# Kernel tuning notes

Hardware: AMD Instinct MI355X
Metric: run time of the kernel (lower is better)

The kernel has to match this reference:

```python
import jax, jax.numpy as jnp
import numpy as np

N = 50000      # nodes
E = 800000     # edges (avg degree 16)
D = 128        # hidden dim
L = 3          # message-passing layers
NU = 1         # DRew nu -> delay = max(k - nu, 0)


def setup_inputs() -> dict:
    key = jax.random.key(0)
    ks = jax.random.split(key, 6)
    x = jax.random.normal(ks[0], (N, D), dtype=jnp.float32)
    edge_index = jax.random.randint(ks[1], (2, E), 0, N)          # [2, E] (src, dst)
    edge_attr = jax.random.randint(ks[2], (E,), 1, L + 1)          # edge types in {1..L}
    scale = 1.0 / np.sqrt(D).astype(np.float32)
    Ws = jax.random.normal(ks[3], (L, D, D), dtype=jnp.float32) * scale       # mlp_s per layer
    bs = jnp.zeros((L, D), dtype=jnp.float32)
    Wk = jax.random.normal(ks[4], (L, L, D, D), dtype=jnp.float32) * scale    # mlp_k, padded; layer t uses k=1..t+1
    bk = jnp.zeros((L, L, D), dtype=jnp.float32)
    eps = jnp.zeros((L,), dtype=jnp.float32)
    return dict(x=x, edge_index=edge_index, edge_attr=edge_attr,
                Ws=Ws, bs=bs, Wk=Wk, bk=bk, eps=eps)


def reference(x, edge_index, edge_attr, Ws, bs, Wk, bk, eps):
    src, dst = edge_index[0], edge_index[1]
    xs = [x]
    for t in range(L):
        xt = xs[-1]
        # out = (1 + eps) * mlp_s(x)
        out = (1.0 + eps[t]) * jax.nn.relu(xt @ Ws[t] + bs[t])
        for k in range(1, t + 2):
            delay = max(k - NU, 0)
            x_src = xs[t - delay]                       # delayed node features
            mask = (edge_attr == k).astype(xt.dtype)    # edge-type mask (replaces boolean column select)
            msg = x_src[src] * mask[:, None]            # gather + mask: [E, D]
            agg = jax.ops.segment_sum(msg, dst, num_segments=N)  # scatter-add per destination
            out = out + jax.nn.relu(agg @ Wk[t, k - 1] + bk[t, k - 1])  # mlp_k(k)
        # gin_nn_post is an empty Sequential -> identity; then F.relu; then residual
        h = jax.nn.relu(out)
        xs.append(xt + h)
    return xs[-1]
```

## Files before the change

kernel.cpp:

```cpp
#include <hip/hip_runtime.h>
#include <hip/hip_bf16.h>


#define NODES 50000
#define EDGES 800000
#define DIM   128
#define ND    ((long)NODES * DIM)
#define NB3   (3 * NODES)
#define NPART 4
#define PSIZE (NODES / NPART)
#define NROWP 50048
#define NBLKS ((NB3 + 255) / 256)

typedef __attribute__((ext_vector_type(8))) short  bf16x8;
typedef __attribute__((ext_vector_type(4))) float  f32x4;

#define LDS_STRIDE 136

__global__ __launch_bounds__(256) void init_kernel(
    const float* __restrict__ x, const float* __restrict__ Ws,
    const float* __restrict__ Wk, __hip_bfloat16* __restrict__ xb0,
    __hip_bfloat16* __restrict__ xb1, __hip_bfloat16* __restrict__ xb2,
    __hip_bfloat16* __restrict__ WT, int* __restrict__ cursor) {
  int b = blockIdx.x, tid = threadIdx.x;
  long i = (long)b * 256 + tid;
  if (i < ND / 4) {
    float4 v = ((const float4*)x)[i];
    union { __hip_bfloat16 h[4]; uint2 u; } pk;
    pk.h[0] = __float2bfloat16(v.x); pk.h[1] = __float2bfloat16(v.y);
    pk.h[2] = __float2bfloat16(v.z); pk.h[3] = __float2bfloat16(v.w);
    ((uint2*)xb0)[i] = pk.u;
  }
  if (b < 12) {
    const float* src = (b < 3) ? (Ws + (long)b * 16384) : (Wk + (long)(b - 3) * 16384);
    __hip_bfloat16* dst = WT + (long)b * 16384;
    for (int idx = tid; idx < 16384; idx += 256) {
      int k = idx >> 7, n = idx & 127;
      dst[n * 128 + k] = __float2bfloat16(src[idx]);
    }
  }
  if (b >= 12 && b < 12 + NBLKS) {
    int g = (b - 12) * 256 + tid;
    if (g < NB3) cursor[g] = 0;
  }
  if (b == 599 && tid < DIM) {
    xb0[(long)NODES * DIM + tid] = __float2bfloat16(0.f);
    xb1[(long)NODES * DIM + tid] = __float2bfloat16(0.f);
    xb2[(long)NODES * DIM + tid] = __float2bfloat16(0.f);
  }
}

__global__ __launch_bounds__(256) void hist_kernel(
    const int* __restrict__ ei, const int* __restrict__ attr,
    int* __restrict__ counts, int E) {
  int e = blockIdx.x * 256 + threadIdx.x;
  if (e >= E) return;
  atomicAdd(&counts[(attr[e] - 1) * NODES + ei[E + e]], 1);
}

__global__ __launch_bounds__(256) void scan_a_kernel(
    const int* __restrict__ counts, int* __restrict__ partial,
    int* __restrict__ blocksums, int n) {
  __shared__ int tmp[256];
  int gid = blockIdx.x * 256 + threadIdx.x;
  int v = (gid < n) ? ((counts[gid] + 3) & ~3) : 0;
  tmp[threadIdx.x] = v;
  __syncthreads();
  for (int off = 1; off < 256; off <<= 1) {
    int t = (threadIdx.x >= off) ? tmp[threadIdx.x - off] : 0;
    __syncthreads();
    tmp[threadIdx.x] += t;
    __syncthreads();
  }
  if (gid < n) partial[gid] = tmp[threadIdx.x] - v;
  if (threadIdx.x == 255) blocksums[blockIdx.x] = tmp[255];
}

__global__ __launch_bounds__(256) void scanc_kernel(
    int* __restrict__ rowptr, int* __restrict__ cursor,
    const int* __restrict__ blocksums, int* __restrict__ csr, int n) {
  __shared__ int red[256];
  int tid = threadIdx.x;
  int partial = 0;
  for (int i = tid; i < blockIdx.x; i += 256) partial += blocksums[i];
  red[tid] = partial;
  __syncthreads();
  for (int off = 128; off > 0; off >>= 1) {
    if (tid < off) red[tid] += red[tid + off];
    __syncthreads();
  }
  int bsoff = red[0];
  int gid = blockIdx.x * 256 + tid;
  if (gid < n) {
    int cnt = cursor[gid];
    int pcnt = (cnt + 3) & ~3;
    int val = rowptr[gid] + bsoff;
    rowptr[gid] = val;
    cursor[gid] = val;
    for (int i = cnt; i < pcnt; ++i) csr[val + i] = NODES;
    if (gid == n - 1) rowptr[n] = val + pcnt;
  }
}

__global__ __launch_bounds__(256) void fill_kernel(
    const int* __restrict__ ei, const int* __restrict__ attr,
    int* __restrict__ cursor, int* __restrict__ csr_src, int E) {
  int p = blockIdx.x & (NPART - 1);
  int chunk = blockIdx.x >> 2;
  int e = chunk * 256 + threadIdx.x;
  if (e >= E) return;
  int d = ei[E + e];
  int lo = p * PSIZE;
  if (d < lo || d >= lo + PSIZE) return;
  int pos = atomicAdd(&cursor[(attr[e] - 1) * NODES + d], 1);
  csr_src[pos] = ei[e];
}

__global__ __launch_bounds__(256, 6) void gather_kernel(
    const __hip_bfloat16* __restrict__ src,
    const int* __restrict__ rowptr, const int* __restrict__ csr,
    __hip_bfloat16* __restrict__ ag0, __hip_bfloat16* __restrict__ ag1,
    __hip_bfloat16* __restrict__ ag2, int nwork) {
  int group = (blockIdx.x * 256 + threadIdx.x) >> 4;
  int lane16 = threadIdx.x & 15;
  if (group >= nwork) return;
  int km1 = (group >= 2 * NODES) ? 2 : ((group >= NODES) ? 1 : 0);
  int d = group - km1 * NODES;
  __hip_bfloat16* ag = (km1 == 0) ? ag0 : ((km1 == 1) ? ag1 : ag2);
  int beg = rowptr[group], end = rowptr[group + 1];
  float a0 = 0.f, a1 = 0.f, a2 = 0.f, a3 = 0.f,
        a4 = 0.f, a5 = 0.f, a6 = 0.f, a7 = 0.f;
  for (int base = beg; base < end; base += 16) {
    int idxv = csr[base + lane16];
    int cnt = end - base; if (cnt > 16) cnt = 16;
    int q0 = __shfl(idxv, 0, 16);
    int q1 = __shfl(idxv, 1, 16);
    int q2 = __shfl(idxv, 2, 16);
    int q3 = __shfl(idxv, 3, 16);
    uint4 v0 = *(const uint4*)(src + (long)q0 * DIM + lane16 * 8);
    uint4 v1 = *(const uint4*)(src + (long)q1 * DIM + lane16 * 8);
    uint4 v2 = *(const uint4*)(src + (long)q2 * DIM + lane16 * 8);
    uint4 v3 = *(const uint4*)(src + (long)q3 * DIM + lane16 * 8);
    for (int j = 0; j < cnt; j += 4) {
      uint4 c0 = v0, c1 = v1, c2 = v2, c3 = v3;
      if (j + 4 < cnt) {
        q0 = __shfl(idxv, j + 4, 16);
        q1 = __shfl(idxv, j + 5, 16);
        q2 = __shfl(idxv, j + 6, 16);
        q3 = __shfl(idxv, j + 7, 16);
        v0 = *(const uint4*)(src + (long)q0 * DIM + lane16 * 8);
        v1 = *(const uint4*)(src + (long)q1 * DIM + lane16 * 8);
        v2 = *(const uint4*)(src + (long)q2 * DIM + lane16 * 8);
        v3 = *(const uint4*)(src + (long)q3 * DIM + lane16 * 8);
      }
      a0 += __uint_as_float(c0.x << 16) + __uint_as_float(c1.x << 16)
          + __uint_as_float(c2.x << 16) + __uint_as_float(c3.x << 16);
      a1 += __uint_as_float(c0.x & 0xffff0000u) + __uint_as_float(c1.x & 0xffff0000u)
          + __uint_as_float(c2.x & 0xffff0000u) + __uint_as_float(c3.x & 0xffff0000u);
      a2 += __uint_as_float(c0.y << 16) + __uint_as_float(c1.y << 16)
          + __uint_as_float(c2.y << 16) + __uint_as_float(c3.y << 16);
      a3 += __uint_as_float(c0.y & 0xffff0000u) + __uint_as_float(c1.y & 0xffff0000u)
          + __uint_as_float(c2.y & 0xffff0000u) + __uint_as_float(c3.y & 0xffff0000u);
      a4 += __uint_as_float(c0.z << 16) + __uint_as_float(c1.z << 16)
          + __uint_as_float(c2.z << 16) + __uint_as_float(c3.z << 16);
      a5 += __uint_as_float(c0.z & 0xffff0000u) + __uint_as_float(c1.z & 0xffff0000u)
          + __uint_as_float(c2.z & 0xffff0000u) + __uint_as_float(c3.z & 0xffff0000u);
      a6 += __uint_as_float(c0.w << 16) + __uint_as_float(c1.w << 16)
          + __uint_as_float(c2.w << 16) + __uint_as_float(c3.w << 16);
      a7 += __uint_as_float(c0.w & 0xffff0000u) + __uint_as_float(c1.w & 0xffff0000u)
          + __uint_as_float(c2.w & 0xffff0000u) + __uint_as_float(c3.w & 0xffff0000u);
    }
  }
  union { __hip_bfloat16 h[8]; uint4 u; } pk;
  pk.h[0] = __float2bfloat16(a0); pk.h[1] = __float2bfloat16(a1);
  pk.h[2] = __float2bfloat16(a2); pk.h[3] = __float2bfloat16(a3);
  pk.h[4] = __float2bfloat16(a4); pk.h[5] = __float2bfloat16(a5);
  pk.h[6] = __float2bfloat16(a6); pk.h[7] = __float2bfloat16(a7);
  *(uint4*)(ag + (long)d * DIM + lane16 * 8) = pk.u;
}

__global__ __launch_bounds__(256, 4) void lgemm_kernel(
    const __hip_bfloat16* __restrict__ xbSelf,
    const __hip_bfloat16* __restrict__ ag0,
    const __hip_bfloat16* __restrict__ ag1,
    const __hip_bfloat16* __restrict__ ag2,
    const __hip_bfloat16* __restrict__ WT,
    const float* __restrict__ bs_t,
    const float* __restrict__ bk_t,
    const float* __restrict__ epsp,
    __hip_bfloat16* __restrict__ xnb,
    float* __restrict__ xn,
    int t) {
  __shared__ __hip_bfloat16 b_lds[128 * LDS_STRIDE];

  int tid = threadIdx.x;
  long row0 = (long)blockIdx.x * 64;
  int wave = tid >> 6, lane = tid & 63;
  int l15 = lane & 15, q = lane >> 4;
  long arow = row0 + wave * 16 + l15;

  const __hip_bfloat16* Asrc[4] = {xbSelf, ag0, ag1, ag2};
  f32x4 out[8];

  for (int p = 0; p <= t + 1; ++p) {
    if (p > 0) __syncthreads();
    const __hip_bfloat16* Am = Asrc[p];
    uint4 af[4];
#pragma unroll
    for (int k0i = 0; k0i < 4; ++k0i)
      af[k0i] = *(const uint4*)(Am + arow * DIM + k0i * 32 + 8 * q);
    const __hip_bfloat16* W = (p == 0) ? (WT + (long)t * 16384)
                                       : (WT + (long)(3 + t * 3 + (p - 1)) * 16384);
    {
      const uint4* bq = (const uint4*)W;
#pragma unroll
      for (int i = 0; i < 8; ++i) {
        int idx = tid + 256 * i;
        int n = idx >> 4, k8 = idx & 15;
        uint4 v = bq[idx];
        *(uint4*)(b_lds + n * LDS_STRIDE + k8 * 8) = v;
      }
    }
    __syncthreads();

    f32x4 acc[8] = {};
#pragma unroll
    for (int k0i = 0; k0i < 4; ++k0i) {
      bf16x8 a = __builtin_bit_cast(bf16x8, af[k0i]);
#pragma unroll
      for (int j = 0; j < 8; ++j) {
        bf16x8 bfr = *(const bf16x8*)(b_lds + (16 * j + l15) * LDS_STRIDE + k0i * 32 + 8 * q);
        acc[j] = __builtin_amdgcn_mfma_f32_16x16x32_bf16(a, bfr, acc[j], 0, 0, 0);
      }
    }
    if (p == 0) {
      float sc = 1.0f + *epsp;
#pragma unroll
      for (int j = 0; j < 8; ++j) {
        float b = bs_t[16 * j + l15];
#pragma unroll
        for (int r = 0; r < 4; ++r) out[j][r] = sc * fmaxf(acc[j][r] + b, 0.f);
      }
    } else {
      const float* bb = bk_t + (p - 1) * 128;
#pragma unroll
      for (int j = 0; j < 8; ++j) {
        float b = bb[16 * j + l15];
#pragma unroll
        for (int r = 0; r < 4; ++r) out[j][r] += fmaxf(acc[j][r] + b, 0.f);
      }
    }
  }

  long rbase = row0 + wave * 16 + q * 4;
  bool fin = (xn != nullptr);
#pragma unroll
  for (int j = 0; j < 8; ++j) {
    int col = 16 * j + l15;
#pragma unroll
    for (int r = 0; r < 4; ++r) {
      long grow = rbase + r;
      if (grow < NODES) {
        float res = __bfloat162float(xbSelf[grow * DIM + col]);
        float v = res + fmaxf(out[j][r], 0.f);
        if (fin) xn[grow * DIM + col] = v;
        else     xnb[grow * DIM + col] = __float2bfloat16(v);
      }
    }
  }
}

extern "C" void kernel_launch(void* const* d_in, const int* in_sizes, int n_in,
                              void* d_out, int out_size, void* d_ws, size_t ws_size,
                              hipStream_t stream) {
  const float* x    = (const float*)d_in[0];
  const int*   ei   = (const int*)d_in[1];
  const int*   attr = (const int*)d_in[2];
  const float* Ws   = (const float*)d_in[3];
  const float* bs   = (const float*)d_in[4];
  const float* Wk   = (const float*)d_in[5];
  const float* bk   = (const float*)d_in[6];
  const float* eps  = (const float*)d_in[7];
  float* out = (float*)d_out;

  char* ws = (char*)d_ws;
  size_t off = 0;
  auto alloc = [&](size_t bytes) { char* p = ws + off; off += (bytes + 255) & ~(size_t)255; return p; };
  const size_t ROWB = (size_t)NROWP * DIM * 2;
  __hip_bfloat16* xb0  = (__hip_bfloat16*)alloc(ROWB);
  __hip_bfloat16* xb1  = (__hip_bfloat16*)alloc(ROWB);
  __hip_bfloat16* xb2  = (__hip_bfloat16*)alloc(ROWB);
  __hip_bfloat16* agA0 = (__hip_bfloat16*)alloc(ROWB);
  __hip_bfloat16* agA1 = (__hip_bfloat16*)alloc(ROWB);
  __hip_bfloat16* agA2 = (__hip_bfloat16*)alloc(ROWB);
  __hip_bfloat16* agB0 = (__hip_bfloat16*)alloc(ROWB);
  __hip_bfloat16* agB1 = (__hip_bfloat16*)alloc(ROWB);
  __hip_bfloat16* agC0 = (__hip_bfloat16*)alloc(ROWB);
  __hip_bfloat16* WT   = (__hip_bfloat16*)alloc(12 * 16384 * 2);
  int* cursor    = (int*)alloc((size_t)NB3 * 4);
  int* rowptr    = (int*)alloc((size_t)(NB3 + 1) * 4 + 256);
  int* blocksums = (int*)alloc(1024 * 4);
  int* csr_src   = (int*)alloc((size_t)(EDGES + 4 * NB3 + 64) * 4);

  int egrid  = (EDGES + 255) / 256;
  int igrid  = (int)(ND / 4 / 256);

  hipLaunchKernelGGL(init_kernel, dim3(igrid), dim3(256), 0, stream,
                     x, Ws, Wk, xb0, xb1, xb2, WT, cursor);
  hipLaunchKernelGGL(hist_kernel, dim3(egrid), dim3(256), 0, stream, ei, attr, cursor, EDGES);
  hipLaunchKernelGGL(scan_a_kernel, dim3(NBLKS), dim3(256), 0, stream, cursor, rowptr, blocksums, NB3);
  hipLaunchKernelGGL(scanc_kernel, dim3(NBLKS), dim3(256), 0, stream,
                     rowptr, cursor, blocksums, csr_src, NB3);
  hipLaunchKernelGGL(fill_kernel, dim3(egrid * NPART), dim3(256), 0, stream, ei, attr, cursor, csr_src, EDGES);

  auto glaunch = [&](int nwork, const __hip_bfloat16* src, __hip_bfloat16* a0,
                     __hip_bfloat16* a1, __hip_bfloat16* a2) {
    int blocks = (nwork * 16 + 255) / 256;
    hipLaunchKernelGGL(gather_kernel, dim3(blocks), dim3(256), 0, stream,
                       src, rowptr, csr_src, a0, a1, a2, nwork);
  };
  int ggrid = (NODES + 63) / 64;

  glaunch(3 * NODES, xb0, agA0, agA1, agA2);
  hipLaunchKernelGGL(lgemm_kernel, dim3(ggrid), dim3(256), 0, stream,
                     xb0, agA0, agA0, agA0, WT, bs + 0, bk + 0, eps + 0,
                     xb1, (float*)nullptr, 0);
  glaunch(2 * NODES, xb1, agB0, agB1, agB1);
  hipLaunchKernelGGL(lgemm_kernel, dim3(ggrid), dim3(256), 0, stream,
                     xb1, agB0, agA1, agA1, WT, bs + 128, bk + 3 * 128, eps + 1,
                     xb2, (float*)nullptr, 1);
  glaunch(NODES, xb2, agC0, agC0, agC0);
  hipLaunchKernelGGL(lgemm_kernel, dim3(ggrid), dim3(256), 0, stream,
                     xb2, agC0, agB1, agA2, WT, bs + 256, bk + 6 * 128, eps + 2,
                     (__hip_bfloat16*)nullptr, out, 2);
}
```

Baseline: 315.8 us.

## Split gather into feature-column passes to keep source slices cache-resident

The neighbour-gather kernel now splits the 128-wide feature dimension into four 32-column passes. Blocks are ordered by pass, and each destination row is handled by 4 lanes instead of 16. During one pass only a 64-byte slice of every source row is touched, so the working set of randomly gathered rows is a quarter as large and has a better chance of staying in L2. In exchange, each gather request moves less data, the edge index list is read four times, and the per-edge loop overhead is repeated per pass.

```diff
diff --git a/kernel.cpp b/kernel.cpp
--- a/kernel.cpp
+++ b/kernel.cpp
@@ -11,6 +11,8 @@
 #define PSIZE (NODES / NPART)
 #define NROWP 50048
 #define NBLKS ((NB3 + 255) / 256)
+#define GNPASS 4
+#define GSLICE 32
 
 typedef __attribute__((ext_vector_type(8))) short  bf16x8;
 typedef __attribute__((ext_vector_type(4))) float  f32x4;
@@ -120,38 +122,44 @@
     const __hip_bfloat16* __restrict__ src,
     const int* __restrict__ rowptr, const int* __restrict__ csr,
     __hip_bfloat16* __restrict__ ag0, __hip_bfloat16* __restrict__ ag1,
-    __hip_bfloat16* __restrict__ ag2, int nwork) {
-  int group = (blockIdx.x * 256 + threadIdx.x) >> 4;
-  int lane16 = threadIdx.x & 15;
+    __hip_bfloat16* __restrict__ ag2, int nwork, int bpp) {
+  int pass = blockIdx.x / bpp;
+  int bin  = blockIdx.x - pass * bpp;
+  int group = bin * 64 + (threadIdx.x >> 2);
+  int lane4 = threadIdx.x & 3;
   if (group >= nwork) return;
   int km1 = (group >= 2 * NODES) ? 2 : ((group >= NODES) ? 1 : 0);
   int d = group - km1 * NODES;
   __hip_bfloat16* ag = (km1 == 0) ? ag0 : ((km1 == 1) ? ag1 : ag2);
+  const __hip_bfloat16* s = src + pass * GSLICE + lane4 * 8;
   int beg = rowptr[group], end = rowptr[group + 1];
   float a0 = 0.f, a1 = 0.f, a2 = 0.f, a3 = 0.f,
         a4 = 0.f, a5 = 0.f, a6 = 0.f, a7 = 0.f;
-  for (int base = beg; base < end; base += 16) {
-    int idxv = csr[base + lane16];
-    int cnt = end - base; if (cnt > 16) cnt = 16;
-    int q0 = __shfl(idxv, 0, 16);
-    int q1 = __shfl(idxv, 1, 16);
-    int q2 = __shfl(idxv, 2, 16);
-    int q3 = __shfl(idxv, 3, 16);
-    uint4 v0 = *(const uint4*)(src + (long)q0 * DIM + lane16 * 8);
-    uint4 v1 = *(const uint4*)(src + (long)q1 * DIM + lane16 * 8);
-    uint4 v2 = *(const uint4*)(src + (long)q2 * DIM + lane16 * 8);
-    uint4 v3 = *(const uint4*)(src + (long)q3 * DIM + lane16 * 8);
-    for (int j = 0; j < cnt; j += 4) {
+  int base = beg;
+  if (base < end) {
+    int idxv = csr[base + lane4];
+    int q0 = __shfl(idxv, 0, 4);
+    int q1 = __shfl(idxv, 1, 4);
+    int q2 = __shfl(idxv, 2, 4);
+    int q3 = __shfl(idxv, 3, 4);
+    uint4 v0 = *(const uint4*)(s + (long)q0 * DIM);
+    uint4 v1 = *(const uint4*)(s + (long)q1 * DIM);
+    uint4 v2 = *(const uint4*)(s + (long)q2 * DIM);
+    uint4 v3 = *(const uint4*)(s + (long)q3 * DIM);
+    for (;;) {
       uint4 c0 = v0, c1 = v1, c2 = v2, c3 = v3;
-      if (j + 4 < cnt) {
-        q0 = __shfl(idxv, j + 4, 16);
-        q1 = __shfl(idxv, j + 5, 16);
-        q2 = __shfl(idxv, j + 6, 16);
-        q3 = __shfl(idxv, j + 7, 16);
-        v0 = *(const uint4*)(src + (long)q0 * DIM + lane16 * 8);
-        v1 = *(const uint4*)(src + (long)q1 * DIM + lane16 * 8);
-        v2 = *(const uint4*)(src + (long)q2 * DIM + lane16 * 8);
-        v3 = *(const uint4*)(src + (long)q3 * DIM + lane16 * 8);
+      base += 4;
+      bool more = (base < end);
+      if (more) {
+        idxv = csr[base + lane4];
+        q0 = __shfl(idxv, 0, 4);
+        q1 = __shfl(idxv, 1, 4);
+        q2 = __shfl(idxv, 2, 4);
+        q3 = __shfl(idxv, 3, 4);
+        v0 = *(const uint4*)(s + (long)q0 * DIM);
+        v1 = *(const uint4*)(s + (long)q1 * DIM);
+        v2 = *(const uint4*)(s + (long)q2 * DIM);
+        v3 = *(const uint4*)(s + (long)q3 * DIM);
       }
       a0 += __uint_as_float(c0.x << 16) + __uint_as_float(c1.x << 16)
           + __uint_as_float(c2.x << 16) + __uint_as_float(c3.x << 16);
@@ -169,6 +177,7 @@
           + __uint_as_float(c2.w << 16) + __uint_as_float(c3.w << 16);
       a7 += __uint_as_float(c0.w & 0xffff0000u) + __uint_as_float(c1.w & 0xffff0000u)
           + __uint_as_float(c2.w & 0xffff0000u) + __uint_as_float(c3.w & 0xffff0000u);
+      if (!more) break;
     }
   }
   union { __hip_bfloat16 h[8]; uint4 u; } pk;
@@ -176,7 +185,7 @@
   pk.h[2] = __float2bfloat16(a2); pk.h[3] = __float2bfloat16(a3);
   pk.h[4] = __float2bfloat16(a4); pk.h[5] = __float2bfloat16(a5);
   pk.h[6] = __float2bfloat16(a6); pk.h[7] = __float2bfloat16(a7);
-  *(uint4*)(ag + (long)d * DIM + lane16 * 8) = pk.u;
+  *(uint4*)(ag + (long)d * DIM + pass * GSLICE + lane4 * 8) = pk.u;
 }
 
 __global__ __launch_bounds__(256, 4) void lgemm_kernel(
@@ -315,9 +324,9 @@
 
   auto glaunch = [&](int nwork, const __hip_bfloat16* src, __hip_bfloat16* a0,
                      __hip_bfloat16* a1, __hip_bfloat16* a2) {
-    int blocks = (nwork * 16 + 255) / 256;
-    hipLaunchKernelGGL(gather_kernel, dim3(blocks), dim3(256), 0, stream,
-                       src, rowptr, csr_src, a0, a1, a2, nwork);
+    int bpp = (nwork + 63) / 64;
+    hipLaunchKernelGGL(gather_kernel, dim3(GNPASS * bpp), dim3(256), 0, stream,
+                       src, rowptr, csr_src, a0, a1, a2, nwork, bpp);
   };
   int ggrid = (NODES + 63) / 64;
 
```

After: 344.7 us. 9.2% more time.

## Fuse graph preprocessing kernels and drop partitioned CSR fill

Applied to the files above, without the earlier changes.

Merges bf16 conversion, weight transpose, pad-row zeroing and the degree histogram into one launch, with a memset clearing the counters. The two-pass scan becomes a single kernel in which each block sums every earlier count itself, and the fill kernel stops splitting destinations into four partitions. The aim is fewer launches and less redundant edge reading. In exchange the scan does redundant quadratic reads over the counts, and the unpartitioned fill loses write locality in the CSR array.

```diff
diff --git a/kernel.cpp b/kernel.cpp
--- a/kernel.cpp
+++ b/kernel.cpp
@@ -7,82 +7,62 @@
 #define DIM   128
 #define ND    ((long)NODES * DIM)
 #define NB3   (3 * NODES)
-#define NPART 4
-#define PSIZE (NODES / NPART)
 #define NROWP 50048
 #define NBLKS ((NB3 + 255) / 256)
+#define EGRID ((EDGES + 255) / 256)
+#define CGRID ((int)(ND / 4 / 256))
 
 typedef __attribute__((ext_vector_type(8))) short  bf16x8;
 typedef __attribute__((ext_vector_type(4))) float  f32x4;
 
 #define LDS_STRIDE 136
 
-__global__ __launch_bounds__(256) void init_kernel(
+__global__ __launch_bounds__(256) void init_hist_kernel(
     const float* __restrict__ x, const float* __restrict__ Ws,
     const float* __restrict__ Wk, __hip_bfloat16* __restrict__ xb0,
     __hip_bfloat16* __restrict__ xb1, __hip_bfloat16* __restrict__ xb2,
-    __hip_bfloat16* __restrict__ WT, int* __restrict__ cursor) {
+    __hip_bfloat16* __restrict__ WT,
+    const int* __restrict__ ei, const int* __restrict__ attr,
+    int* __restrict__ cursor) {
   int b = blockIdx.x, tid = threadIdx.x;
-  long i = (long)b * 256 + tid;
-  if (i < ND / 4) {
+  if (b < CGRID) {
+    long i = (long)b * 256 + tid;
     float4 v = ((const float4*)x)[i];
     union { __hip_bfloat16 h[4]; uint2 u; } pk;
     pk.h[0] = __float2bfloat16(v.x); pk.h[1] = __float2bfloat16(v.y);
     pk.h[2] = __float2bfloat16(v.z); pk.h[3] = __float2bfloat16(v.w);
     ((uint2*)xb0)[i] = pk.u;
-  }
-  if (b < 12) {
-    const float* src = (b < 3) ? (Ws + (long)b * 16384) : (Wk + (long)(b - 3) * 16384);
-    __hip_bfloat16* dst = WT + (long)b * 16384;
+  } else if (b < CGRID + 12) {
+    int wb = b - CGRID;
+    const float* src = (wb < 3) ? (Ws + (long)wb * 16384) : (Wk + (long)(wb - 3) * 16384);
+    __hip_bfloat16* dst = WT + (long)wb * 16384;
     for (int idx = tid; idx < 16384; idx += 256) {
       int k = idx >> 7, n = idx & 127;
       dst[n * 128 + k] = __float2bfloat16(src[idx]);
     }
-  }
-  if (b >= 12 && b < 12 + NBLKS) {
-    int g = (b - 12) * 256 + tid;
-    if (g < NB3) cursor[g] = 0;
-  }
-  if (b == 599 && tid < DIM) {
-    xb0[(long)NODES * DIM + tid] = __float2bfloat16(0.f);
-    xb1[(long)NODES * DIM + tid] = __float2bfloat16(0.f);
-    xb2[(long)NODES * DIM + tid] = __float2bfloat16(0.f);
-  }
-}
-
-__global__ __launch_bounds__(256) void hist_kernel(
-    const int* __restrict__ ei, const int* __restrict__ attr,
-    int* __restrict__ counts, int E) {
-  int e = blockIdx.x * 256 + threadIdx.x;
-  if (e >= E) return;
-  atomicAdd(&counts[(attr[e] - 1) * NODES + ei[E + e]], 1);
-}
-
-__global__ __launch_bounds__(256) void scan_a_kernel(
-    const int* __restrict__ counts, int* __restrict__ partial,
-    int* __restrict__ blocksums, int n) {
+  } else if (b < CGRID + 14) {
+    int g = (b - (CGRID + 12)) * 256 + tid;
+    if (g < 3 * DIM) {
+      int which = g >> 7, dcol = g & 127;
+      __hip_bfloat16* xb = (which == 0) ? xb0 : ((which == 1) ? xb1 : xb2);
+      xb[(long)NODES * DIM + dcol] = __float2bfloat16(0.f);
+    }
+  } else {
+    int e = (b - (CGRID + 14)) * 256 + tid;
+    if (e < EDGES)
+      atomicAdd(&cursor[(attr[e] - 1) * NODES + ei[EDGES + e]], 1);
+  }
+}
+
+__global__ __launch_bounds__(256) void scan_kernel(
+    const int* __restrict__ cursor, int* __restrict__ rowptr,
+    int* __restrict__ cur2, int* __restrict__ csr, int n) {
+  __shared__ int red[256];
   __shared__ int tmp[256];
-  int gid = blockIdx.x * 256 + threadIdx.x;
-  int v = (gid < n) ? ((counts[gid] + 3) & ~3) : 0;
-  tmp[threadIdx.x] = v;
-  __syncthreads();
-  for (int off = 1; off < 256; off <<= 1) {
-    int t = (threadIdx.x >= off) ? tmp[threadIdx.x - off] : 0;
-    __syncthreads();
-    tmp[threadIdx.x] += t;
-    __syncthreads();
-  }
-  if (gid < n) partial[gid] = tmp[threadIdx.x] - v;
-  if (threadIdx.x == 255) blocksums[blockIdx.x] = tmp[255];
-}
-
-__global__ __launch_bounds__(256) void scanc_kernel(
-    int* __restrict__ rowptr, int* __restrict__ cursor,
-    const int* __restrict__ blocksums, int* __restrict__ csr, int n) {
-  __shared__ int red[256];
   int tid = threadIdx.x;
+  int limit = blockIdx.x * 256;
   int partial = 0;
-  for (int i = tid; i < blockIdx.x; i += 256) partial += blocksums[i];
+  for (int i = tid; i < limit; i += 256) partial += (cursor[i] + 3) & ~3;
   red[tid] = partial;
   __syncthreads();
   for (int off = 128; off > 0; off >>= 1) {
@@ -90,29 +70,32 @@
     __syncthreads();
   }
   int bsoff = red[0];
-  int gid = blockIdx.x * 256 + tid;
+  int gid = limit + tid;
+  int cnt = (gid < n) ? cursor[gid] : 0;
+  int pv = (cnt + 3) & ~3;
+  tmp[tid] = pv;
+  __syncthreads();
+  for (int off = 1; off < 256; off <<= 1) {
+    int t = (tid >= off) ? tmp[tid - off] : 0;
+    __syncthreads();
+    tmp[tid] += t;
+    __syncthreads();
+  }
   if (gid < n) {
-    int cnt = cursor[gid];
-    int pcnt = (cnt + 3) & ~3;
-    int val = rowptr[gid] + bsoff;
+    int val = tmp[tid] - pv + bsoff;
     rowptr[gid] = val;
-    cursor[gid] = val;
-    for (int i = cnt; i < pcnt; ++i) csr[val + i] = NODES;
-    if (gid == n - 1) rowptr[n] = val + pcnt;
+    cur2[gid] = val;
+    for (int i = cnt; i < pv; ++i) csr[val + i] = NODES;
+    if (gid == n - 1) rowptr[n] = val + pv;
   }
 }
 
 __global__ __launch_bounds__(256) void fill_kernel(
     const int* __restrict__ ei, const int* __restrict__ attr,
-    int* __restrict__ cursor, int* __restrict__ csr_src, int E) {
-  int p = blockIdx.x & (NPART - 1);
-  int chunk = blockIdx.x >> 2;
-  int e = chunk * 256 + threadIdx.x;
+    int* __restrict__ cur2, int* __restrict__ csr_src, int E) {
+  int e = blockIdx.x * 256 + threadIdx.x;
   if (e >= E) return;
-  int d = ei[E + e];
-  int lo = p * PSIZE;
-  if (d < lo || d >= lo + PSIZE) return;
-  int pos = atomicAdd(&cursor[(attr[e] - 1) * NODES + d], 1);
+  int pos = atomicAdd(&cur2[(attr[e] - 1) * NODES + ei[E + e]], 1);
   csr_src[pos] = ei[e];
 }
 
@@ -298,20 +281,17 @@
   __hip_bfloat16* agC0 = (__hip_bfloat16*)alloc(ROWB);
   __hip_bfloat16* WT   = (__hip_bfloat16*)alloc(12 * 16384 * 2);
   int* cursor    = (int*)alloc((size_t)NB3 * 4);
+  int* cur2      = (int*)alloc((size_t)NB3 * 4);
   int* rowptr    = (int*)alloc((size_t)(NB3 + 1) * 4 + 256);
-  int* blocksums = (int*)alloc(1024 * 4);
   int* csr_src   = (int*)alloc((size_t)(EDGES + 4 * NB3 + 64) * 4);
 
-  int egrid  = (EDGES + 255) / 256;
-  int igrid  = (int)(ND / 4 / 256);
-
-  hipLaunchKernelGGL(init_kernel, dim3(igrid), dim3(256), 0, stream,
-                     x, Ws, Wk, xb0, xb1, xb2, WT, cursor);
-  hipLaunchKernelGGL(hist_kernel, dim3(egrid), dim3(256), 0, stream, ei, attr, cursor, EDGES);
-  hipLaunchKernelGGL(scan_a_kernel, dim3(NBLKS), dim3(256), 0, stream, cursor, rowptr, blocksums, NB3);
-  hipLaunchKernelGGL(scanc_kernel, dim3(NBLKS), dim3(256), 0, stream,
-                     rowptr, cursor, blocksums, csr_src, NB3);
-  hipLaunchKernelGGL(fill_kernel, dim3(egrid * NPART), dim3(256), 0, stream, ei, attr, cursor, csr_src, EDGES);
+  hipMemsetAsync(cursor, 0, (size_t)NB3 * 4, stream);
+  hipLaunchKernelGGL(init_hist_kernel, dim3(CGRID + 14 + EGRID), dim3(256), 0, stream,
+                     x, Ws, Wk, xb0, xb1, xb2, WT, ei, attr, cursor);
+  hipLaunchKernelGGL(scan_kernel, dim3(NBLKS), dim3(256), 0, stream,
+                     cursor, rowptr, cur2, csr_src, NB3);
+  hipLaunchKernelGGL(fill_kernel, dim3(EGRID), dim3(256), 0, stream,
+                     ei, attr, cur2, csr_src, EDGES);
 
   auto glaunch = [&](int nwork, const __hip_bfloat16* src, __hip_bfloat16* a0,
                      __hip_bfloat16* a1, __hip_bfloat16* a2) {
```

Result: slower. 394.8 us (+25.0%).
